# Kernel optimization log

Measured on AMD Instinct MI355X. Metric: run time of the kernel, lower is better.

The kernel has to match this reference:

```python
import jax, jax.numpy as jnp
import numpy as np

N = 100000
E = 640000
IN, HID, OUT = 128, 256, 128


def _glorot(key, shape):
    fan_in, fan_out = shape[0], shape[1]
    lim = (6.0 / (fan_in + fan_out)) ** 0.5
    return jax.random.uniform(key, shape, jnp.float32, -lim, lim)


def setup_inputs() -> dict:
    key = jax.random.key(0)
    ks = jax.random.split(key, 8)
    x = jax.random.normal(ks[0], (N, IN), jnp.float32)
    edge_index = jax.random.randint(ks[1], (2, E), 0, N, jnp.int64)
    # conv0 MLP: in->hid->hid
    w0a = _glorot(ks[2], (IN, HID)); b0a = jnp.zeros((HID,), jnp.float32)
    w0b = _glorot(ks[3], (HID, HID)); b0b = jnp.zeros((HID,), jnp.float32)
    # conv1 MLP: hid->hid->hid
    w1a = _glorot(ks[4], (HID, HID)); b1a = jnp.zeros((HID,), jnp.float32)
    w1b = _glorot(ks[5], (HID, HID)); b1b = jnp.zeros((HID,), jnp.float32)
    # conv2 MLP: hid->out->out
    w2a = _glorot(ks[6], (HID, OUT)); b2a = jnp.zeros((OUT,), jnp.float32)
    w2b = _glorot(ks[7], (OUT, OUT)); b2b = jnp.zeros((OUT,), jnp.float32)
    return dict(x=x, edge_index=edge_index,
                w0a=w0a, b0a=b0a, w0b=w0b, b0b=b0b,
                w1a=w1a, b1a=b1a, w1b=w1b, b1b=b1b,
                w2a=w2a, b2a=b2a, w2b=w2b, b2b=b2b)


def reference(x, edge_index, w0a, b0a, w0b, b0b, w1a, b1a, w1b, b1b, w2a, b2a, w2b, b2b):
    src, dst = edge_index[0], edge_index[1]
    n = x.shape[0]
    layers = [(w0a, b0a, w0b, b0b), (w1a, b1a, w1b, b1b), (w2a, b2a, w2b, b2b)]
    for wa, ba, wb, bb in layers:
        # GINConv (eps=0): aggregate neighbor messages x[src] into dst, add self
        agg = jax.ops.segment_sum(x[src], dst, num_segments=n)  # [N, d]
        h = x + agg
        h = jnp.maximum(h @ wa + ba, 0.0) @ wb + bb  # MLP: Linear-ReLU-Linear
        x = jnp.maximum(h, 0.0)  # outer F.relu
    return x
```

## Files before the change

### kernel.cpp

```cpp
#include <hip/hip_runtime.h>
#include <hip/hip_bf16.h>

typedef __attribute__((ext_vector_type(4))) float f32x4;
typedef __attribute__((ext_vector_type(8))) short short8;
typedef unsigned short u16;

__device__ inline float bf2f(u16 u) {
    unsigned int x = ((unsigned int)u) << 16;
    return __builtin_bit_cast(float, x);
}
__device__ inline u16 f2bf(float f) {
    unsigned int x = __builtin_bit_cast(unsigned int, f);
    unsigned int r = (x + 0x7FFFu + ((x >> 16) & 1u)) >> 16;
    return (u16)r;
}

__device__ inline int edge_at(const void* edges, int flag64, long long idx) {
    if (flag64) return (int)((const long long*)edges)[idx];
    return ((const int*)edges)[idx];
}

__global__ void probe_kernel(const void* edges, int n, int* flag) {
    if (threadIdx.x == 0 && blockIdx.x == 0) {
        const long long* p = (const long long*)edges;
        int ok = 1;
        for (int i = 0; i < 64; ++i) {
            long long v = p[i];
            if (v < 0 || v >= n) { ok = 0; break; }
        }
        *flag = ok;
    }
}

__global__ void hist_kernel(const void* edges, const int* flag, int E, int* deg) {
    int f = *flag;
    for (long long i = blockIdx.x * blockDim.x + threadIdx.x; i < E;
         i += (long long)gridDim.x * blockDim.x) {
        int dst = edge_at(edges, f, (long long)E + i);
        atomicAdd(&deg[dst], 1);
    }
}

__global__ void scan1_kernel(const int* deg, int* incl, int* bsum, int n) {
    __shared__ int s[256];
    int i = blockIdx.x * 256 + threadIdx.x;
    int v = (i < n) ? deg[i] : 0;
    s[threadIdx.x] = v;
    __syncthreads();
    for (int d = 1; d < 256; d <<= 1) {
        int t = (threadIdx.x >= d) ? s[threadIdx.x - d] : 0;
        __syncthreads();
        s[threadIdx.x] += t;
        __syncthreads();
    }
    if (i < n) incl[i] = s[threadIdx.x];
    if (threadIdx.x == 255) bsum[blockIdx.x] = s[255];
}

__global__ void scan2_kernel(const int* bsum, int* boff, int nb) {
    __shared__ int s[512];
    int t = threadIdx.x;
    int v = (t < nb) ? bsum[t] : 0;
    s[t] = v;
    __syncthreads();
    for (int d = 1; d < 512; d <<= 1) {
        int u = (t >= d) ? s[t - d] : 0;
        __syncthreads();
        s[t] += u;
        __syncthreads();
    }
    boff[t] = s[t] - v;
}

__global__ void scan3_kernel(const int* incl, const int* deg, const int* boff,
                             int* offs, int* cursor, int n, int E) {
    int i = blockIdx.x * 256 + threadIdx.x;
    if (i < n) {
        int o = boff[blockIdx.x] + incl[i] - deg[i];
        offs[i] = o;
        cursor[i] = o;
    }
    if (i == 0) offs[n] = E;
}

__global__ void scatter_kernel(const void* edges, const int* flag, int E,
                               int* cursor, int* nbr) {
    int f = *flag;
    for (long long i = blockIdx.x * blockDim.x + threadIdx.x; i < E;
         i += (long long)gridDim.x * blockDim.x) {
        int src = edge_at(edges, f, i);
        int dst = edge_at(edges, f, (long long)E + i);
        int pos = atomicAdd(&cursor[dst], 1);
        nbr[pos] = src;
    }
}

__global__ void cvt_x_kernel(const float* __restrict__ x, u16* __restrict__ out, long long n4) {
    long long i = blockIdx.x * blockDim.x + threadIdx.x;
    if (i >= n4) return;
    float4 v = ((const float4*)x)[i];
    ushort4 o;
    o.x = f2bf(v.x); o.y = f2bf(v.y); o.z = f2bf(v.z); o.w = f2bf(v.w);
    ((ushort4*)out)[i] = o;
}

__global__ void cvt_w_kernel(const float* __restrict__ W, u16* __restrict__ Wt, int K, int M) {
    int i = blockIdx.x * blockDim.x + threadIdx.x;
    if (i >= K * M) return;
    int m = i / K, k = i % K;
    Wt[i] = f2bf(W[(size_t)k * M + m]);
}

template <int FP>
__global__ __launch_bounds__(64) void agg_kernel(
    const u16* __restrict__ X, u16* __restrict__ H,
    const int* __restrict__ offs, const int* __restrict__ nbr, int n, int d) {
    const int node = blockIdx.x;
    const int lane = threadIdx.x;
    float acc[FP];
    const u16* xr = X + (size_t)node * d + lane * FP;
    if (FP == 2) {
        ushort2 v = *(const ushort2*)xr;
        acc[0] = bf2f(v.x); acc[1] = bf2f(v.y);
    } else {
        ushort4 v = *(const ushort4*)xr;
        acc[0] = bf2f(v.x); acc[1] = bf2f(v.y); acc[2] = bf2f(v.z); acc[3] = bf2f(v.w);
    }
    const int s = offs[node], e = offs[node + 1];
    int j = s;
    for (; j + 4 <= e; j += 4) {
        int n0 = nbr[j], n1 = nbr[j + 1], n2 = nbr[j + 2], n3 = nbr[j + 3];
        if (FP == 2) {
            ushort2 v0 = *(const ushort2*)(X + (size_t)n0 * d + lane * 2);
            ushort2 v1 = *(const ushort2*)(X + (size_t)n1 * d + lane * 2);
            ushort2 v2 = *(const ushort2*)(X + (size_t)n2 * d + lane * 2);
            ushort2 v3 = *(const ushort2*)(X + (size_t)n3 * d + lane * 2);
            acc[0] += bf2f(v0.x) + bf2f(v1.x) + bf2f(v2.x) + bf2f(v3.x);
            acc[1] += bf2f(v0.y) + bf2f(v1.y) + bf2f(v2.y) + bf2f(v3.y);
        } else {
            ushort4 v0 = *(const ushort4*)(X + (size_t)n0 * d + lane * 4);
            ushort4 v1 = *(const ushort4*)(X + (size_t)n1 * d + lane * 4);
            ushort4 v2 = *(const ushort4*)(X + (size_t)n2 * d + lane * 4);
            ushort4 v3 = *(const ushort4*)(X + (size_t)n3 * d + lane * 4);
            acc[0] += bf2f(v0.x) + bf2f(v1.x) + bf2f(v2.x) + bf2f(v3.x);
            acc[1] += bf2f(v0.y) + bf2f(v1.y) + bf2f(v2.y) + bf2f(v3.y);
            acc[2] += bf2f(v0.z) + bf2f(v1.z) + bf2f(v2.z) + bf2f(v3.z);
            acc[3] += bf2f(v0.w) + bf2f(v1.w) + bf2f(v2.w) + bf2f(v3.w);
        }
    }
    for (; j < e; ++j) {
        int nb = nbr[j];
        if (FP == 2) {
            ushort2 v = *(const ushort2*)(X + (size_t)nb * d + lane * 2);
            acc[0] += bf2f(v.x); acc[1] += bf2f(v.y);
        } else {
            ushort4 v = *(const ushort4*)(X + (size_t)nb * d + lane * 4);
            acc[0] += bf2f(v.x); acc[1] += bf2f(v.y); acc[2] += bf2f(v.z); acc[3] += bf2f(v.w);
        }
    }
    u16* hr = H + (size_t)node * d + lane * FP;
    if (FP == 2) {
        ushort2 o; o.x = f2bf(acc[0]); o.y = f2bf(acc[1]);
        *(ushort2*)hr = o;
    } else {
        ushort4 o; o.x = f2bf(acc[0]); o.y = f2bf(acc[1]); o.z = f2bf(acc[2]); o.w = f2bf(acc[3]);
        *(ushort4*)hr = o;
    }
}

__device__ inline f32x4 mfma16(short8 a, short8 b, f32x4 c) {
    return __builtin_amdgcn_mfma_f32_16x16x32_bf16(a, b, c, 0, 0, 0);
}

template <int K1, int M1, int M2, bool F32OUT>
__global__ __launch_bounds__(256, 3) void mlp_kernel(
    const u16* __restrict__ H,
    const u16* __restrict__ W1t,
    const float* __restrict__ b1,
    const u16* __restrict__ W2t,
    const float* __restrict__ b2,
    void* __restrict__ outp,
    int Nrows) {
    constexpr int S1 = K1 + 8;
    constexpr int S2 = M1 + 8;
    constexpr int SO = M2 + 8;
    constexpr int OB = F32OUT ? 4 : 2;
    constexpr int CF1 = M1 / 64, CF2 = M2 / 64;
    constexpr int NK1 = K1 / 32, NK2 = M1 / 32;
    constexpr size_t LB1 = (size_t)64 * S1 * 2, LB2 = (size_t)64 * S2 * 2;
    constexpr size_t LBO = (size_t)64 * SO * OB;
    constexpr size_t LB = LB1 > LB2 ? (LB1 > LBO ? LB1 : LBO) : (LB2 > LBO ? LB2 : LBO);
    __shared__ __align__(16) char smem[LB];
    u16* bufA = (u16*)smem;
    u16* bufT = (u16*)smem;

    const int r0 = blockIdx.x * 64;
    const int tid = threadIdx.x;
    const int lane = tid & 63;
    const int wid = tid >> 6;
    const int fl = lane & 15;
    const int kg = lane >> 4;
    const int rb = kg << 2;

    {
        constexpr int TPR = K1 / 8;
        constexpr int RPI = 256 / TPR;
        const int rr = tid / TPR;
        const int ce = (tid % TPR) * 8;
#pragma unroll
        for (int it = 0; it < 64 / RPI; ++it) {
            const int row = it * RPI + rr;
            uint4 v = make_uint4(0, 0, 0, 0);
            if (r0 + row < Nrows) v = *(const uint4*)(H + (size_t)(r0 + row) * K1 + ce);
            *(uint4*)&bufA[row * S1 + ce] = v;
        }
    }
    __syncthreads();

    f32x4 acc1[4][CF1];
#pragma unroll
    for (int m = 0; m < 4; ++m)
#pragma unroll
        for (int c = 0; c < CF1; ++c) acc1[m][c] = (f32x4){0.f, 0.f, 0.f, 0.f};

    const int slab1 = wid * (M1 / 4);
    const u16* wp1[CF1];
#pragma unroll
    for (int c = 0; c < CF1; ++c)
        wp1[c] = W1t + (size_t)(slab1 + c * 16 + fl) * K1 + kg * 8;

    {
        short8 bc[CF1], bn[CF1];
#pragma unroll
        for (int c = 0; c < CF1; ++c) bc[c] = *(const short8*)wp1[c];
#pragma unroll
        for (int kk = 0; kk < NK1; ++kk) {
            if (kk + 1 < NK1) {
#pragma unroll
                for (int c = 0; c < CF1; ++c)
                    bn[c] = *(const short8*)(wp1[c] + (kk + 1) * 32);
            }
            short8 a[4];
#pragma unroll
            for (int m = 0; m < 4; ++m)
                a[m] = *(const short8*)&bufA[(m * 16 + fl) * S1 + kk * 32 + kg * 8];
#pragma unroll
            for (int c = 0; c < CF1; ++c)
#pragma unroll
                for (int m = 0; m < 4; ++m) acc1[m][c] = mfma16(a[m], bc[c], acc1[m][c]);
#pragma unroll
            for (int c = 0; c < CF1; ++c) bc[c] = bn[c];
        }
    }
    __syncthreads();

#pragma unroll
    for (int c = 0; c < CF1; ++c) {
        const int col = slab1 + c * 16 + fl;
        const float bias = b1[col];
#pragma unroll
        for (int m = 0; m < 4; ++m)
#pragma unroll
            for (int j = 0; j < 4; ++j) {
                float v = fmaxf(acc1[m][c][j] + bias, 0.f);
                bufT[(m * 16 + rb + j) * S2 + col] = f2bf(v);
            }
    }
    __syncthreads();

    f32x4 acc2[4][CF2];
#pragma unroll
    for (int m = 0; m < 4; ++m)
#pragma unroll
        for (int c = 0; c < CF2; ++c) acc2[m][c] = (f32x4){0.f, 0.f, 0.f, 0.f};

    const int slab2 = wid * (M2 / 4);
    const u16* wp2[CF2];
#pragma unroll
    for (int c = 0; c < CF2; ++c)
        wp2[c] = W2t + (size_t)(slab2 + c * 16 + fl) * M1 + kg * 8;

    {
        short8 bc[CF2], bn[CF2];
#pragma unroll
        for (int c = 0; c < CF2; ++c) bc[c] = *(const short8*)wp2[c];
#pragma unroll
        for (int kk = 0; kk < NK2; ++kk) {
            if (kk + 1 < NK2) {
#pragma unroll
                for (int c = 0; c < CF2; ++c)
                    bn[c] = *(const short8*)(wp2[c] + (kk + 1) * 32);
            }
            short8 a[4];
#pragma unroll
            for (int m = 0; m < 4; ++m)
                a[m] = *(const short8*)&bufT[(m * 16 + fl) * S2 + kk * 32 + kg * 8];
#pragma unroll
            for (int c = 0; c < CF2; ++c)
#pragma unroll
                for (int m = 0; m < 4; ++m) acc2[m][c] = mfma16(a[m], bc[c], acc2[m][c]);
#pragma unroll
            for (int c = 0; c < CF2; ++c) bc[c] = bn[c];
        }
    }
    __syncthreads();

#pragma unroll
    for (int c = 0; c < CF2; ++c) {
        const int col = slab2 + c * 16 + fl;
        const float bias = b2[col];
#pragma unroll
        for (int m = 0; m < 4; ++m)
#pragma unroll
            for (int j = 0; j < 4; ++j) {
                float v = fmaxf(acc2[m][c][j] + bias, 0.f);
                const int row = m * 16 + rb + j;
                if (F32OUT)
                    ((float*)smem)[row * SO + col] = v;
                else
                    ((u16*)smem)[row * SO + col] = f2bf(v);
            }
    }
    __syncthreads();

    {
        constexpr int ROWB = M2 * OB;
        constexpr int TPRO = ROWB / 16;
        constexpr int RPIO = 256 / TPRO;
        const int rr = tid / TPRO;
        const int cb = (tid % TPRO) * 16;
#pragma unroll
        for (int it = 0; it < 64 / RPIO; ++it) {
            const int row = it * RPIO + rr;
            if (r0 + row < Nrows) {
                uint4 v = *(const uint4*)(smem + (size_t)row * SO * OB + cb);
                *(uint4*)((char*)outp + (size_t)(r0 + row) * ROWB + cb) = v;
            }
        }
    }
}

extern "C" void kernel_launch(void* const* d_in, const int* in_sizes, int n_in,
                              void* d_out, int out_size, void* d_ws, size_t ws_size,
                              hipStream_t stream) {
    const int IN = 128, HID = 256, OUTD = 128;
    const int N = in_sizes[0] / IN;
    const int E = in_sizes[1] / 2;

    const float* x = (const float*)d_in[0];
    const void* edges = d_in[1];
    const float* w0a = (const float*)d_in[2];  const float* b0a = (const float*)d_in[3];
    const float* w0b = (const float*)d_in[4];  const float* b0b = (const float*)d_in[5];
    const float* w1a = (const float*)d_in[6];  const float* b1a = (const float*)d_in[7];
    const float* w1b = (const float*)d_in[8];  const float* b1b = (const float*)d_in[9];
    const float* w2a = (const float*)d_in[10]; const float* b2a = (const float*)d_in[11];
    const float* w2b = (const float*)d_in[12]; const float* b2b = (const float*)d_in[13];

    char* ws = (char*)d_ws;
    size_t off = 0;
    auto alloc = [&](size_t b) { size_t o = off; off = (off + b + 255) & ~(size_t)255; return o; };
    int* flag   = (int*)(ws + alloc(4));
    int* deg    = (int*)(ws + alloc((size_t)N * 4));
    int* incl   = (int*)(ws + alloc((size_t)N * 4));
    int* bsum   = (int*)(ws + alloc(512 * 4));
    int* boff   = (int*)(ws + alloc(512 * 4));
    int* offs   = (int*)(ws + alloc((size_t)(N + 1) * 4));
    int* cursor = (int*)(ws + alloc((size_t)N * 4));
    int* nbr    = (int*)(ws + alloc((size_t)E * 4));
    u16* wt0a = (u16*)(ws + alloc((size_t)IN * HID * 2));
    u16* wt0b = (u16*)(ws + alloc((size_t)HID * HID * 2));
    u16* wt1a = (u16*)(ws + alloc((size_t)HID * HID * 2));
    u16* wt1b = (u16*)(ws + alloc((size_t)HID * HID * 2));
    u16* wt2a = (u16*)(ws + alloc((size_t)HID * OUTD * 2));
    u16* wt2b = (u16*)(ws + alloc((size_t)OUTD * OUTD * 2));
    u16* Pa = (u16*)(ws + alloc((size_t)N * HID * 2));
    u16* Pb = (u16*)(ws + alloc((size_t)N * HID * 2));

    probe_kernel<<<1, 64, 0, stream>>>(edges, N, flag);
    hipMemsetAsync(deg, 0, (size_t)N * 4, stream);
    hist_kernel<<<2048, 256, 0, stream>>>(edges, flag, E, deg);
    int nb1 = (N + 255) / 256;
    scan1_kernel<<<nb1, 256, 0, stream>>>(deg, incl, bsum, N);
    scan2_kernel<<<1, 512, 0, stream>>>(bsum, boff, nb1);
    scan3_kernel<<<nb1, 256, 0, stream>>>(incl, deg, boff, offs, cursor, N, E);
    scatter_kernel<<<2048, 256, 0, stream>>>(edges, flag, E, cursor, nbr);

    long long n4 = (long long)N * IN / 4;
    cvt_x_kernel<<<(int)((n4 + 255) / 256), 256, 0, stream>>>(x, Pa, n4);
    cvt_w_kernel<<<(IN * HID + 255) / 256, 256, 0, stream>>>(w0a, wt0a, IN, HID);
    cvt_w_kernel<<<(HID * HID + 255) / 256, 256, 0, stream>>>(w0b, wt0b, HID, HID);
    cvt_w_kernel<<<(HID * HID + 255) / 256, 256, 0, stream>>>(w1a, wt1a, HID, HID);
    cvt_w_kernel<<<(HID * HID + 255) / 256, 256, 0, stream>>>(w1b, wt1b, HID, HID);
    cvt_w_kernel<<<(HID * OUTD + 255) / 256, 256, 0, stream>>>(w2a, wt2a, HID, OUTD);
    cvt_w_kernel<<<(OUTD * OUTD + 255) / 256, 256, 0, stream>>>(w2b, wt2b, OUTD, OUTD);

    const int nblk = (N + 63) / 64;
    agg_kernel<2><<<N, 64, 0, stream>>>(Pa, Pb, offs, nbr, N, IN);
    mlp_kernel<128, 256, 256, false><<<nblk, 256, 0, stream>>>(Pb, wt0a, b0a, wt0b, b0b, Pa, N);
    agg_kernel<4><<<N, 64, 0, stream>>>(Pa, Pb, offs, nbr, N, HID);
    mlp_kernel<256, 256, 256, false><<<nblk, 256, 0, stream>>>(Pb, wt1a, b1a, wt1b, b1b, Pa, N);
    agg_kernel<4><<<N, 64, 0, stream>>>(Pa, Pb, offs, nbr, N, HID);
    mlp_kernel<256, 128, 128, true><<<nblk, 256, 0, stream>>>(Pb, wt2a, b2a, wt2b, b2b, d_out, N);
}
```

Before: 410.2 us.

## Make MLP kernel persistent with register-resident weights and prefetched row tiles

The fused MLP kernel becomes a persistent grid of up to 512 blocks with 512 threads (8 waves). Each wave loads its slice of both weight matrices and biases into registers once, instead of streaming weights from global memory for every 64-row tile. The next tile's input rows are prefetched into registers while the current tile computes. This cuts repeated weight traffic and launch overhead, but raises register pressure considerably (e.g. 8x16 short8 weight fragments for K1=256), which risks spills or low occupancy.

```diff
diff --git a/kernel.cpp b/kernel.cpp
--- a/kernel.cpp
+++ b/kernel.cpp
@@ -173,28 +173,28 @@
 }
 
 template <int K1, int M1, int M2, bool F32OUT>
-__global__ __launch_bounds__(256, 3) void mlp_kernel(
+__global__ __launch_bounds__(512, 2) void mlp_kernel(
     const u16* __restrict__ H,
     const u16* __restrict__ W1t,
     const float* __restrict__ b1,
     const u16* __restrict__ W2t,
     const float* __restrict__ b2,
     void* __restrict__ outp,
-    int Nrows) {
+    int Nrows, int ntiles) {
     constexpr int S1 = K1 + 8;
     constexpr int S2 = M1 + 8;
-    constexpr int SO = M2 + 8;
+    constexpr int SO = F32OUT ? (M2 + 4) : (M2 + 8);
     constexpr int OB = F32OUT ? 4 : 2;
-    constexpr int CF1 = M1 / 64, CF2 = M2 / 64;
     constexpr int NK1 = K1 / 32, NK2 = M1 / 32;
-    constexpr size_t LB1 = (size_t)64 * S1 * 2, LB2 = (size_t)64 * S2 * 2;
-    constexpr size_t LBO = (size_t)64 * SO * OB;
-    constexpr size_t LB = LB1 > LB2 ? (LB1 > LBO ? LB1 : LBO) : (LB2 > LBO ? LB2 : LBO);
+    constexpr int CW1 = M1 / 128, CW2 = M2 / 128;
+    constexpr size_t LA = (size_t)64 * S1 * 2;
+    constexpr size_t LT = (size_t)64 * S2 * 2;
+    constexpr size_t LO = (size_t)64 * SO * OB;
+    constexpr size_t LB = LA > LT ? (LA > LO ? LA : LO) : (LT > LO ? LT : LO);
     __shared__ __align__(16) char smem[LB];
     u16* bufA = (u16*)smem;
     u16* bufT = (u16*)smem;
 
-    const int r0 = blockIdx.x * 64;
     const int tid = threadIdx.x;
     const int lane = tid & 63;
     const int wid = tid >> 6;
@@ -202,141 +202,137 @@
     const int kg = lane >> 4;
     const int rb = kg << 2;
 
-    {
-        constexpr int TPR = K1 / 8;
-        constexpr int RPI = 256 / TPR;
-        const int rr = tid / TPR;
-        const int ce = (tid % TPR) * 8;
-#pragma unroll
-        for (int it = 0; it < 64 / RPI; ++it) {
-            const int row = it * RPI + rr;
-            uint4 v = make_uint4(0, 0, 0, 0);
-            if (r0 + row < Nrows) v = *(const uint4*)(H + (size_t)(r0 + row) * K1 + ce);
-            *(uint4*)&bufA[row * S1 + ce] = v;
-        }
-    }
-    __syncthreads();
-
-    f32x4 acc1[4][CF1];
-#pragma unroll
-    for (int m = 0; m < 4; ++m)
-#pragma unroll
-        for (int c = 0; c < CF1; ++c) acc1[m][c] = (f32x4){0.f, 0.f, 0.f, 0.f};
-
-    const int slab1 = wid * (M1 / 4);
-    const u16* wp1[CF1];
-#pragma unroll
-    for (int c = 0; c < CF1; ++c)
-        wp1[c] = W1t + (size_t)(slab1 + c * 16 + fl) * K1 + kg * 8;
-
-    {
-        short8 bc[CF1], bn[CF1];
-#pragma unroll
-        for (int c = 0; c < CF1; ++c) bc[c] = *(const short8*)wp1[c];
+    const int ws1 = wid * (M1 / 8);
+    const int ws2 = wid * (M2 / 8);
+    short8 w1f[CW1][NK1];
+    short8 w2f[CW2][NK2];
+    float bias1[CW1], bias2[CW2];
+#pragma unroll
+    for (int c = 0; c < CW1; ++c) {
+        const u16* wp = W1t + (size_t)(ws1 + c * 16 + fl) * K1 + kg * 8;
+        bias1[c] = b1[ws1 + c * 16 + fl];
+#pragma unroll
+        for (int kk = 0; kk < NK1; ++kk) w1f[c][kk] = *(const short8*)(wp + kk * 32);
+    }
+#pragma unroll
+    for (int c = 0; c < CW2; ++c) {
+        const u16* wp = W2t + (size_t)(ws2 + c * 16 + fl) * M1 + kg * 8;
+        bias2[c] = b2[ws2 + c * 16 + fl];
+#pragma unroll
+        for (int kk = 0; kk < NK2; ++kk) w2f[c][kk] = *(const short8*)(wp + kk * 32);
+    }
+
+    constexpr int TPR = K1 / 8;
+    constexpr int RPI = 512 / TPR;
+    constexpr int NPASS = 64 / RPI;
+    const int srow = tid / TPR;
+    const int sce = (tid % TPR) * 8;
+
+    uint4 apf[NPASS];
+    auto load_tile = [&](int t) {
+#pragma unroll
+        for (int p = 0; p < NPASS; ++p) {
+            apf[p] = make_uint4(0, 0, 0, 0);
+            if (t < ntiles) {
+                const int r = t * 64 + p * RPI + srow;
+                if (r < Nrows) apf[p] = *(const uint4*)(H + (size_t)r * K1 + sce);
+            }
+        }
+    };
+
+    load_tile(blockIdx.x);
+
+    for (int t = blockIdx.x; t < ntiles; t += gridDim.x) {
+        const int r0 = t * 64;
+#pragma unroll
+        for (int p = 0; p < NPASS; ++p)
+            *(uint4*)&bufA[(p * RPI + srow) * S1 + sce] = apf[p];
+        __syncthreads();
+
+        load_tile(t + gridDim.x);
+
+        f32x4 acc[4][CW1];
+#pragma unroll
+        for (int m = 0; m < 4; ++m)
+#pragma unroll
+            for (int c = 0; c < CW1; ++c) acc[m][c] = (f32x4){0.f, 0.f, 0.f, 0.f};
 #pragma unroll
         for (int kk = 0; kk < NK1; ++kk) {
-            if (kk + 1 < NK1) {
-#pragma unroll
-                for (int c = 0; c < CF1; ++c)
-                    bn[c] = *(const short8*)(wp1[c] + (kk + 1) * 32);
-            }
             short8 a[4];
 #pragma unroll
             for (int m = 0; m < 4; ++m)
                 a[m] = *(const short8*)&bufA[(m * 16 + fl) * S1 + kk * 32 + kg * 8];
 #pragma unroll
-            for (int c = 0; c < CF1; ++c)
-#pragma unroll
-                for (int m = 0; m < 4; ++m) acc1[m][c] = mfma16(a[m], bc[c], acc1[m][c]);
-#pragma unroll
-            for (int c = 0; c < CF1; ++c) bc[c] = bn[c];
-        }
-    }
-    __syncthreads();
-
-#pragma unroll
-    for (int c = 0; c < CF1; ++c) {
-        const int col = slab1 + c * 16 + fl;
-        const float bias = b1[col];
+            for (int c = 0; c < CW1; ++c)
+#pragma unroll
+                for (int m = 0; m < 4; ++m) acc[m][c] = mfma16(a[m], w1f[c][kk], acc[m][c]);
+        }
+        __syncthreads();
+
+#pragma unroll
+        for (int c = 0; c < CW1; ++c) {
+            const int col = ws1 + c * 16 + fl;
+#pragma unroll
+            for (int m = 0; m < 4; ++m)
+#pragma unroll
+                for (int j = 0; j < 4; ++j) {
+                    float v = fmaxf(acc[m][c][j] + bias1[c], 0.f);
+                    bufT[(m * 16 + rb + j) * S2 + col] = f2bf(v);
+                }
+        }
+        __syncthreads();
+
+        f32x4 acc2[4][CW2];
 #pragma unroll
         for (int m = 0; m < 4; ++m)
 #pragma unroll
-            for (int j = 0; j < 4; ++j) {
-                float v = fmaxf(acc1[m][c][j] + bias, 0.f);
-                bufT[(m * 16 + rb + j) * S2 + col] = f2bf(v);
-            }
-    }
-    __syncthreads();
-
-    f32x4 acc2[4][CF2];
-#pragma unroll
-    for (int m = 0; m < 4; ++m)
-#pragma unroll
-        for (int c = 0; c < CF2; ++c) acc2[m][c] = (f32x4){0.f, 0.f, 0.f, 0.f};
-
-    const int slab2 = wid * (M2 / 4);
-    const u16* wp2[CF2];
-#pragma unroll
-    for (int c = 0; c < CF2; ++c)
-        wp2[c] = W2t + (size_t)(slab2 + c * 16 + fl) * M1 + kg * 8;
-
-    {
-        short8 bc[CF2], bn[CF2];
-#pragma unroll
-        for (int c = 0; c < CF2; ++c) bc[c] = *(const short8*)wp2[c];
+            for (int c = 0; c < CW2; ++c) acc2[m][c] = (f32x4){0.f, 0.f, 0.f, 0.f};
 #pragma unroll
         for (int kk = 0; kk < NK2; ++kk) {
-            if (kk + 1 < NK2) {
-#pragma unroll
-                for (int c = 0; c < CF2; ++c)
-                    bn[c] = *(const short8*)(wp2[c] + (kk + 1) * 32);
-            }
             short8 a[4];
 #pragma unroll
             for (int m = 0; m < 4; ++m)
                 a[m] = *(const short8*)&bufT[(m * 16 + fl) * S2 + kk * 32 + kg * 8];
 #pragma unroll
-            for (int c = 0; c < CF2; ++c)
-#pragma unroll
-                for (int m = 0; m < 4; ++m) acc2[m][c] = mfma16(a[m], bc[c], acc2[m][c]);
-#pragma unroll
-            for (int c = 0; c < CF2; ++c) bc[c] = bn[c];
-        }
-    }
-    __syncthreads();
-
-#pragma unroll
-    for (int c = 0; c < CF2; ++c) {
-        const int col = slab2 + c * 16 + fl;
-        const float bias = b2[col];
-#pragma unroll
-        for (int m = 0; m < 4; ++m)
-#pragma unroll
-            for (int j = 0; j < 4; ++j) {
-                float v = fmaxf(acc2[m][c][j] + bias, 0.f);
-                const int row = m * 16 + rb + j;
-                if (F32OUT)
-                    ((float*)smem)[row * SO + col] = v;
-                else
-                    ((u16*)smem)[row * SO + col] = f2bf(v);
+            for (int c = 0; c < CW2; ++c)
+#pragma unroll
+                for (int m = 0; m < 4; ++m) acc2[m][c] = mfma16(a[m], w2f[c][kk], acc2[m][c]);
+        }
+        __syncthreads();
+
+#pragma unroll
+        for (int c = 0; c < CW2; ++c) {
+            const int col = ws2 + c * 16 + fl;
+#pragma unroll
+            for (int m = 0; m < 4; ++m)
+#pragma unroll
+                for (int j = 0; j < 4; ++j) {
+                    float v = fmaxf(acc2[m][c][j] + bias2[c], 0.f);
+                    const int row = m * 16 + rb + j;
+                    if (F32OUT)
+                        ((float*)smem)[row * SO + col] = v;
+                    else
+                        ((u16*)smem)[row * SO + col] = f2bf(v);
+                }
+        }
+        __syncthreads();
+
+        {
+            constexpr int ROWB = M2 * OB;
+            constexpr int TPRO = ROWB / 16;
+            constexpr int RPIO = 512 / TPRO;
+            const int orow = tid / TPRO;
+            const int ocb = (tid % TPRO) * 16;
+#pragma unroll
+            for (int p = 0; p < 64 / RPIO; ++p) {
+                const int row = p * RPIO + orow;
+                if (r0 + row < Nrows) {
+                    uint4 v = *(const uint4*)(smem + (size_t)row * SO * OB + ocb);
+                    *(uint4*)((char*)outp + (size_t)(r0 + row) * ROWB + ocb) = v;
+                }
             }
-    }
-    __syncthreads();
-
-    {
-        constexpr int ROWB = M2 * OB;
-        constexpr int TPRO = ROWB / 16;
-        constexpr int RPIO = 256 / TPRO;
-        const int rr = tid / TPRO;
-        const int cb = (tid % TPRO) * 16;
-#pragma unroll
-        for (int it = 0; it < 64 / RPIO; ++it) {
-            const int row = it * RPIO + rr;
-            if (r0 + row < Nrows) {
-                uint4 v = *(const uint4*)(smem + (size_t)row * SO * OB + cb);
-                *(uint4*)((char*)outp + (size_t)(r0 + row) * ROWB + cb) = v;
-            }
-        }
+        }
+        __syncthreads();
     }
 }
 
@@ -394,11 +390,13 @@
     cvt_w_kernel<<<(HID * OUTD + 255) / 256, 256, 0, stream>>>(w2a, wt2a, HID, OUTD);
     cvt_w_kernel<<<(OUTD * OUTD + 255) / 256, 256, 0, stream>>>(w2b, wt2b, OUTD, OUTD);
 
-    const int nblk = (N + 63) / 64;
+    const int ntiles = (N + 63) / 64;
+    const int mgrid = ntiles < 512 ? ntiles : 512;
+
     agg_kernel<2><<<N, 64, 0, stream>>>(Pa, Pb, offs, nbr, N, IN);
-    mlp_kernel<128, 256, 256, false><<<nblk, 256, 0, stream>>>(Pb, wt0a, b0a, wt0b, b0b, Pa, N);
+    mlp_kernel<128, 256, 256, false><<<mgrid, 512, 0, stream>>>(Pb, wt0a, b0a, wt0b, b0b, Pa, N, ntiles);
     agg_kernel<4><<<N, 64, 0, stream>>>(Pa, Pb, offs, nbr, N, HID);
-    mlp_kernel<256, 256, 256, false><<<nblk, 256, 0, stream>>>(Pb, wt1a, b1a, wt1b, b1b, Pa, N);
+    mlp_kernel<256, 256, 256, false><<<mgrid, 512, 0, stream>>>(Pb, wt1a, b1a, wt1b, b1b, Pa, N, ntiles);
     agg_kernel<4><<<N, 64, 0, stream>>>(Pa, Pb, offs, nbr, N, HID);
-    mlp_kernel<256, 128, 128, true><<<nblk, 256, 0, stream>>>(Pb, wt2a, b2a, wt2b, b2b, d_out, N);
-}
+    mlp_kernel<256, 128, 128, true><<<mgrid, 512, 0, stream>>>(Pb, wt2a, b2a, wt2b, b2b, d_out, N, ntiles);
+}
```

Measured after the change: 371.5 us. -9.4%, faster.
